# Kernel optimization log

Measured on AMD Instinct MI355X. Metric: run time of the kernel, lower is better.

Reference implementation:

```python
import jax, jax.numpy as jnp
import numpy as np
import math

B, S, D, H, HD, P = 2, 2048, 2048, 16, 128, 10
ROPE_BASE = 10000.0


def _rope_tables(seq_len, head_dim):
    inv_freq = 1.0 / (ROPE_BASE ** (np.arange(0, head_dim, 2, dtype=np.float32) / head_dim))
    t = np.arange(seq_len, dtype=np.float32)
    freqs = np.outer(t, inv_freq)                  # [S, hd/2]
    emb = np.concatenate([freqs, freqs], axis=-1)  # [S, hd]
    return jnp.asarray(np.cos(emb)), jnp.asarray(np.sin(emb))


def _rotate_half(x):
    half = x.shape[-1] // 2
    return jnp.concatenate([-x[..., half:], x[..., :half]], axis=-1)


def setup_inputs() -> dict:
    key = jax.random.key(0)
    ks = jax.random.split(key, 8)
    hidden_states = jax.random.normal(ks[0], (B, S, D), dtype=jnp.float32)
    # causal additive mask, llama convention: 0 where allowed, large negative above diagonal
    causal = jnp.triu(jnp.full((S, S), -1e9, dtype=jnp.float32), k=1)
    attention_mask = jnp.broadcast_to(causal[None, None], (B, 1, S, S))
    position_ids = jnp.broadcast_to(jnp.arange(S, dtype=jnp.int64)[None], (B, S))
    scale = 1.0 / math.sqrt(D)
    Wq = jax.random.normal(ks[1], (D, D), dtype=jnp.float32) * scale
    Wk = jax.random.normal(ks[2], (D, D), dtype=jnp.float32) * scale
    Wv = jax.random.normal(ks[3], (D, D), dtype=jnp.float32) * scale
    Wo = jax.random.normal(ks[4], (D, D), dtype=jnp.float32) * scale
    adapter_query = jax.random.normal(ks[5], (P, D), dtype=jnp.float32)
    adapter_gate = jax.random.normal(ks[6], (1, H, 1, 1), dtype=jnp.float32) * 0.1
    return dict(hidden_states=hidden_states, attention_mask=attention_mask,
                position_ids=position_ids, Wq=Wq, Wk=Wk, Wv=Wv, Wo=Wo,
                adapter_query=adapter_query, adapter_gate=adapter_gate)


def reference(hidden_states, attention_mask, position_ids, Wq, Wk, Wv, Wo,
              adapter_query, adapter_gate):
    bsz, q_len, _ = hidden_states.shape
    inv_sqrt_hd = 1.0 / math.sqrt(HD)

    def split_heads(x):  # [B,S,D] -> [B,H,S,hd]
        return x.reshape(bsz, q_len, H, HD).transpose(0, 2, 1, 3)

    q = split_heads(hidden_states @ Wq)
    k = split_heads(hidden_states @ Wk)
    v = split_heads(hidden_states @ Wv)

    # RoPE
    cos_t, sin_t = _rope_tables(q_len, HD)
    cos = cos_t[position_ids][:, None]  # [B,1,S,hd]
    sin = sin_t[position_ids][:, None]
    q = q * cos + _rotate_half(q) * sin
    k = k * cos + _rotate_half(k) * sin

    # main attention
    scores = jnp.einsum('bhqd,bhkd->bhqk', q, k) * inv_sqrt_hd
    scores = scores + attention_mask
    attn = jax.nn.softmax(scores.astype(jnp.float32), axis=-1).astype(q.dtype)
    attn_out = jnp.einsum('bhqk,bhkd->bhqd', attn, v)

    # adapter: soft prompt projected through k/v proj (learn_kv=False), no RoPE
    adapter = jnp.broadcast_to(adapter_query[None], (bsz, P, D))  # [B,P,D]
    a_k = (adapter @ Wk).reshape(bsz, P, H, HD).transpose(0, 2, 1, 3)  # [B,H,P,hd]
    a_v = (adapter @ Wv).reshape(bsz, P, H, HD).transpose(0, 2, 1, 3)
    a_scores = jnp.einsum('bhqd,bhpd->bhqp', q, a_k) * inv_sqrt_hd
    a_w = adapter_gate * jax.nn.softmax(a_scores.astype(jnp.float32), axis=-1).astype(q.dtype)
    a_out = jnp.einsum('bhqp,bhpd->bhqd', a_w, a_v)

    out = attn_out + a_out
    out = out.transpose(0, 2, 1, 3).reshape(bsz, q_len, D)
    return out @ Wo
```

## Files before the change

### kernel.cpp

```cpp
#include <hip/hip_runtime.h>
#include <cstdint>
#include <cstddef>

typedef __bf16 bf16x8 __attribute__((ext_vector_type(8)));
typedef float  f32x4  __attribute__((ext_vector_type(4)));

__device__ __forceinline__ unsigned short f2bf(float f) {
  unsigned int u = __float_as_uint(f);
  u += 0x7FFF + ((u >> 16) & 1);
  return (unsigned short)(u >> 16);
}
__device__ __forceinline__ float bf2f(unsigned short u) {
  return __uint_as_float(((unsigned int)u) << 16);
}

#define SEQ 2048
#define DMODEL 2048
#define NH 16
#define HD 128
#define NB 2
#define NP 10
#define MAUG 4106
#define SCALEL2 (0.08838834764831845f * 1.44269504088896340f)

#define GLOAD_LDS16(g, l) \
  __builtin_amdgcn_global_load_lds((__attribute__((address_space(1))) const void*)(g), \
                                   (__attribute__((address_space(3))) void*)(l), 16, 0, 0)

#define FENCE() asm volatile("" ::: "memory")
#define SBAR() do { FENCE(); __builtin_amdgcn_s_barrier(); FENCE(); } while (0)
#define WAITVM(N) asm volatile("s_waitcnt vmcnt(" #N ")" ::: "memory")

__global__ void k_tables(float* __restrict__ cost, float* __restrict__ sint) {
  int idx = blockIdx.x * 256 + threadIdx.x;
  if (idx >= SEQ * 64) return;
  int s = idx >> 6, i = idx & 63;
  double invf = exp(-((double)(2 * i) / 128.0) * log(10000.0));
  double a = (double)s * invf;
  float c = (float)cos(a), sn = (float)sin(a);
  cost[s * HD + i] = c;  cost[s * HD + 64 + i] = c;
  sint[s * HD + i] = sn; sint[s * HD + 64 + i] = sn;
}

__global__ __launch_bounds__(256) void k_wt(const float* __restrict__ W0,
                                            const float* __restrict__ W1,
                                            const float* __restrict__ W2,
                                            const float* __restrict__ W3,
                                            unsigned short* __restrict__ out) {
  __shared__ float tile[32][33];
  const float* W = (blockIdx.z == 0) ? W0 : (blockIdx.z == 1) ? W1 : (blockIdx.z == 2) ? W2 : W3;
  unsigned short* o = out + (size_t)blockIdx.z * DMODEL * DMODEL;
  int bx = blockIdx.x * 32, by = blockIdx.y * 32;
  int tx = threadIdx.x & 31, ty = threadIdx.x >> 5;
  #pragma unroll
  for (int j = 0; j < 32; j += 8)
    tile[ty + j][tx] = W[(size_t)(bx + ty + j) * DMODEL + by + tx];
  __syncthreads();
  #pragma unroll
  for (int j = 0; j < 32; j += 8)
    o[(size_t)(by + ty + j) * DMODEL + bx + tx] = f2bf(tile[tx][ty + j]);
}

__global__ void k_xaug(const float* __restrict__ X, const float* __restrict__ Aq,
                       unsigned short* __restrict__ xaug) {
  size_t idx = (size_t)blockIdx.x * 256 + threadIdx.x;
  if (idx >= (size_t)MAUG * DMODEL) return;
  size_t row = idx >> 11;
  int col = (int)(idx & 2047);
  float v = (row < (size_t)NB * SEQ) ? X[idx] : Aq[(row - NB * SEQ) * DMODEL + col];
  xaug[idx] = f2bf(v);
}

#define RD_A(dst, bb, MH) do { \
  _Pragma("unroll") for (int i_ = 0; i_ < 4; i_++) \
    _Pragma("unroll") for (int ks_ = 0; ks_ < 2; ks_++) \
      dst[i_][ks_] = *(const bf16x8*)&lds[(bb) + (wr*128 + (MH)*64 + i_*16 + lr)*64 + (((ks_*4+quad) ^ (lr & 7)) * 8)]; \
} while (0)

#define RD_B(dst, bb, NHH) do { \
  _Pragma("unroll") for (int j_ = 0; j_ < 2; j_++) \
    _Pragma("unroll") for (int ks_ = 0; ks_ < 2; ks_++) \
      dst[j_][ks_] = *(const bf16x8*)&lds[(bb) + 16384 + (wc*64 + (NHH)*32 + j_*16 + lr)*64 + (((ks_*4+quad) ^ (lr & 7)) * 8)]; \
} while (0)

#define MM(A, B, MH, NHH) do { \
  __builtin_amdgcn_s_setprio(1); \
  _Pragma("unroll") for (int i_ = 0; i_ < 4; i_++) \
    _Pragma("unroll") for (int j_ = 0; j_ < 2; j_++) { \
      acc[(MH)*4+i_][(NHH)*2+j_] = __builtin_amdgcn_mfma_f32_16x16x32_bf16(A[i_][0], B[j_][0], acc[(MH)*4+i_][(NHH)*2+j_], 0, 0, 0); \
      acc[(MH)*4+i_][(NHH)*2+j_] = __builtin_amdgcn_mfma_f32_16x16x32_bf16(A[i_][1], B[j_][1], acc[(MH)*4+i_][(NHH)*2+j_], 0, 0, 0); \
    } \
  __builtin_amdgcn_s_setprio(0); \
} while (0)

#define STG_AE(nb, ko) do { \
  GLOAD_LDS16(sA + (ko),                      &lds[(nb)*32768 + (qrow)*64 + g8]); \
  GLOAD_LDS16(sA + 128*(size_t)DMODEL + (ko), &lds[(nb)*32768 + (128+qrow)*64 + g8]); } while (0)
#define STG_AO(nb, ko) do { \
  GLOAD_LDS16(sA + 64*(size_t)DMODEL + (ko),  &lds[(nb)*32768 + (64+qrow)*64 + g8]); \
  GLOAD_LDS16(sA + 192*(size_t)DMODEL + (ko), &lds[(nb)*32768 + (192+qrow)*64 + g8]); } while (0)
#define STG_BE(nb, ko) do { \
  GLOAD_LDS16(sB + (ko),                      &lds[(nb)*32768 + 16384 + (qb)*64 + g8]); \
  GLOAD_LDS16(sB + 128*(size_t)DMODEL + (ko), &lds[(nb)*32768 + 16384 + (128+qb)*64 + g8]); } while (0)
#define STG_BO(nb, ko) do { \
  GLOAD_LDS16(sB + 32*(size_t)DMODEL + (ko),  &lds[(nb)*32768 + 16384 + (32+qb)*64 + g8]); \
  GLOAD_LDS16(sB + 160*(size_t)DMODEL + (ko), &lds[(nb)*32768 + 16384 + (160+qb)*64 + g8]); } while (0)

template<int BF16OUT>
__global__ __launch_bounds__(512, 2) void k_gemm256(const unsigned short* __restrict__ A,
                                                    const unsigned short* __restrict__ Bt,
                                                    void* __restrict__ Cv,
                                                    int M, size_t c_stride_mat) {
  __shared__ unsigned short lds[65536];
  const int t = threadIdx.x;
  const int lane = t & 63, w = t >> 6;
  const int lr = lane & 15, quad = lane >> 4;
  const int wr = w >> 2, wc = w & 3;
  const int tm = (M + 255) >> 8;
  const int perz = tm * 8;
  const int qchunk = gridDim.x >> 3;
  const int lin = ((int)blockIdx.x & 7) * qchunk + ((int)blockIdx.x >> 3);
  const int z = lin / perz;
  const int rem = lin - z * perz;
  const int m0 = (rem >> 3) * 256, n0 = (rem & 7) * 256;
  const unsigned short* Bz = Bt + (size_t)z * DMODEL * DMODEL;

  const int qrow = t >> 3;
  const int g8 = (t & 7) * 8;
  const int gsw8 = (((t & 7) ^ (qrow & 7)) * 8);
  const int qb = (qrow < 32) ? qrow : qrow + 32;

  const unsigned short* sA = A + (size_t)(m0 + qrow) * DMODEL + gsw8;
  const unsigned short* sB = Bz + (size_t)(n0 + qb) * DMODEL + gsw8;

  bf16x8 aE[4][2], aO[4][2], bE[2][2], bO[2][2];
  f32x4 acc[8][4];
  #pragma unroll
  for (int i = 0; i < 8; i++)
    #pragma unroll
    for (int j = 0; j < 4; j++) acc[i][j] = (f32x4){0.f, 0.f, 0.f, 0.f};

  STG_AE(0, 0); STG_BE(0, 0); STG_BO(0, 0); STG_AO(0, 0);
  WAITVM(4);
  SBAR();
  RD_A(aE, 0, 0); RD_B(bE, 0, 0);

  for (int kt = 0; kt < DMODEL / 64; kt++) {
    const int base = (kt & 1) << 15;
    const int nb2 = (kt & 1) ^ 1;
    const int nbase = nb2 << 15;
    const int ko = (kt + 1) * 64;
    const bool more = (kt + 1 < DMODEL / 64);

    if (more) { STG_AE(nb2, ko); WAITVM(4); } else WAITVM(2);
    SBAR();
    RD_B(bO, base, 1);
    MM(aE, bE, 0, 0);

    if (more) { STG_BE(nb2, ko); WAITVM(4); } else WAITVM(0);
    SBAR();
    RD_A(aO, base, 1);
    MM(aE, bO, 0, 1);

    if (more) STG_BO(nb2, ko);
    MM(aO, bE, 1, 0);

    if (more) {
      STG_AO(nb2, ko);
      WAITVM(4);
      SBAR();
      RD_A(aE, nbase, 0); RD_B(bE, nbase, 0);
    }
    MM(aO, bO, 1, 1);
  }

  #pragma unroll
  for (int mi = 0; mi < 8; mi++) {
    #pragma unroll
    for (int r = 0; r < 4; r++) {
      int row = m0 + wr * 128 + mi * 16 + quad * 4 + r;
      if (row < M) {
        if (BF16OUT) {
          unsigned short* C = (unsigned short*)Cv + (size_t)z * c_stride_mat;
          #pragma unroll
          for (int n = 0; n < 4; n++)
            C[(size_t)row * DMODEL + n0 + wc * 64 + n * 16 + lr] = f2bf(acc[mi][n][r]);
        } else {
          float* C = (float*)Cv + (size_t)z * c_stride_mat;
          #pragma unroll
          for (int n = 0; n < 4; n++)
            C[(size_t)row * DMODEL + n0 + wc * 64 + n * 16 + lr] = acc[mi][n][r];
        }
      }
    }
  }
}

#define O_LDA(MH) do { \
  _Pragma("unroll") for (int i_ = 0; i_ < 2; i_++) \
    _Pragma("unroll") for (int ks_ = 0; ks_ < 2; ks_++) \
      a[i_][ks_] = *(const bf16x8*)&lds[base + (wr*64 + ((MH)*2+i_)*16 + lr)*64 + (((ks_*4+quad) ^ (lr & 7)) * 8)]; \
} while (0)

#define O_LDB(NHH) do { \
  _Pragma("unroll") for (int j_ = 0; j_ < 2; j_++) \
    _Pragma("unroll") for (int ks_ = 0; ks_ < 2; ks_++) \
      b[(NHH)*2+j_][ks_] = *(const bf16x8*)&lds[base + 8192 + (wc*64 + ((NHH)*2+j_)*16 + lr)*64 + (((ks_*4+quad) ^ (lr & 7)) * 8)]; \
} while (0)

#define O_MFMA(MH, NHH) do { \
  __builtin_amdgcn_s_setprio(1); \
  _Pragma("unroll") for (int i_ = 0; i_ < 2; i_++) \
    _Pragma("unroll") for (int j_ = 0; j_ < 2; j_++) { \
      acc[(MH)*2+i_][(NHH)*2+j_] = __builtin_amdgcn_mfma_f32_16x16x32_bf16(a[i_][0], b[(NHH)*2+j_][0], acc[(MH)*2+i_][(NHH)*2+j_], 0, 0, 0); \
      acc[(MH)*2+i_][(NHH)*2+j_] = __builtin_amdgcn_mfma_f32_16x16x32_bf16(a[i_][1], b[(NHH)*2+j_][1], acc[(MH)*2+i_][(NHH)*2+j_], 0, 0, 0); \
    } \
  __builtin_amdgcn_s_setprio(0); \
} while (0)

#define O_STG_AE(nb, ko) GLOAD_LDS16(sA + (ko), &lds[(nb)*24576 + (qb)*64 + g8])
#define O_STG_AO(nb, ko) GLOAD_LDS16(sA + 32*(size_t)DMODEL + (ko), &lds[(nb)*24576 + (32+qb)*64 + g8])
#define O_STG_BE(nb, ko) do { \
  GLOAD_LDS16(sB + (ko),                      &lds[(nb)*24576 + 8192 + (qb)*64 + g8]); \
  GLOAD_LDS16(sB + 128*(size_t)DMODEL + (ko), &lds[(nb)*24576 + 8192 + (128+qb)*64 + g8]); } while (0)
#define O_STG_BO(nb, ko) do { \
  GLOAD_LDS16(sB + 32*(size_t)DMODEL + (ko),  &lds[(nb)*24576 + 8192 + (32+qb)*64 + g8]); \
  GLOAD_LDS16(sB + 160*(size_t)DMODEL + (ko), &lds[(nb)*24576 + 8192 + (160+qb)*64 + g8]); } while (0)

__global__ __launch_bounds__(512, 2) void k_gemmo(const unsigned short* __restrict__ A,
                                                  const unsigned short* __restrict__ Bt,
                                                  float* __restrict__ C) {
  __shared__ unsigned short lds[49152];
  const int t = threadIdx.x;
  const int lane = t & 63, w = t >> 6;
  const int lr = lane & 15, quad = lane >> 4;
  const int wr = w >> 2, wc = w & 3;
  const int lin = ((int)blockIdx.x & 7) * 32 + ((int)blockIdx.x >> 3);
  const int m0 = (lin >> 3) * 128, n0 = (lin & 7) * 256;

  const int qrow = t >> 3;
  const int g8 = (t & 7) * 8;
  const int gsw8 = (((t & 7) ^ (qrow & 7)) * 8);
  const int qb = (qrow < 32) ? qrow : qrow + 32;

  const unsigned short* sA = A + (size_t)(m0 + qb) * DMODEL + gsw8;
  const unsigned short* sB = Bt + (size_t)(n0 + qb) * DMODEL + gsw8;

  bf16x8 a[2][2], b[4][2];
  f32x4 acc[4][4];
  #pragma unroll
  for (int i = 0; i < 4; i++)
    #pragma unroll
    for (int j = 0; j < 4; j++) acc[i][j] = (f32x4){0.f, 0.f, 0.f, 0.f};

  O_STG_AE(0, 0); O_STG_BE(0, 0); O_STG_BO(0, 0); O_STG_AO(0, 0);
  WAITVM(3);
  SBAR();

  for (int kt = 0; kt < DMODEL / 64; kt++) {
    const int base = (kt & 1) * 24576;
    const int nb = (kt & 1) ^ 1;
    const int ko = (kt + 1) * 64;
    const bool more = (kt + 1 < DMODEL / 64);

    O_LDA(0);
    O_LDB(0);
    if (more) O_STG_AE(nb, ko);
    SBAR();
    O_MFMA(0, 0);
    if (more) WAITVM(2); else WAITVM(1);
    SBAR();

    O_LDB(1);
    if (more) O_STG_BE(nb, ko);
    SBAR();
    O_MFMA(0, 1);
    if (more) WAITVM(3); else WAITVM(0);
    SBAR();

    O_LDA(1);
    if (more) O_STG_BO(nb, ko);
    SBAR();
    O_MFMA(1, 0);
    SBAR();

    if (more) O_STG_AO(nb, ko);
    SBAR();
    O_MFMA(1, 1);
    if (more) WAITVM(3);
    SBAR();
  }

  #pragma unroll
  for (int mi = 0; mi < 4; mi++) {
    #pragma unroll
    for (int r = 0; r < 4; r++) {
      int row = m0 + wr * 64 + mi * 16 + quad * 4 + r;
      #pragma unroll
      for (int n = 0; n < 4; n++)
        C[(size_t)row * DMODEL + n0 + wc * 64 + n * 16 + lr] = acc[mi][n][r];
    }
  }
}

__global__ __launch_bounds__(256) void k_rope(const unsigned short* __restrict__ Qf,
                                              const unsigned short* __restrict__ Kf,
                                              const unsigned short* __restrict__ Vf,
                                              const float* __restrict__ cost, const float* __restrict__ sint,
                                              unsigned short* __restrict__ Qb, unsigned short* __restrict__ Kb,
                                              unsigned short* __restrict__ AKb, unsigned short* __restrict__ avt) {
  int row = blockIdx.x;
  int t = threadIdx.x;
  int c0 = t * 8;
  size_t off = (size_t)row * DMODEL + c0;
  if (row < NB * SEQ) {
    int s = row & (SEQ - 1);
    int d0 = c0 & (HD - 1);
    int po = (d0 < 64) ? 64 : -64;
    float sign = (d0 < 64) ? -1.f : 1.f;
    uint4 qv = *(const uint4*)&Qf[off];
    uint4 qp = *(const uint4*)&Qf[off + po];
    uint4 kv = *(const uint4*)&Kf[off];
    uint4 kp = *(const uint4*)&Kf[off + po];
    const unsigned short* qa = (const unsigned short*)&qv;
    const unsigned short* qb2 = (const unsigned short*)&qp;
    const unsigned short* ka = (const unsigned short*)&kv;
    const unsigned short* kb2 = (const unsigned short*)&kp;
    unsigned short oq[8], ok[8];
    #pragma unroll
    for (int j = 0; j < 8; j++) {
      float cv = cost[s * HD + d0 + j], sv = sint[s * HD + d0 + j];
      oq[j] = f2bf(bf2f(qa[j]) * cv + sign * bf2f(qb2[j]) * sv);
      ok[j] = f2bf(bf2f(ka[j]) * cv + sign * bf2f(kb2[j]) * sv);
    }
    *(uint4*)&Qb[off] = *(const uint4*)oq;
    *(uint4*)&Kb[off] = *(const uint4*)ok;
  } else {
    int p = row - NB * SEQ;
    uint4 kv = *(const uint4*)&Kf[off];
    uint4 vv = *(const uint4*)&Vf[off];
    *(uint4*)&AKb[(size_t)p * DMODEL + c0] = kv;
    const unsigned short* vp = (const unsigned short*)&vv;
    #pragma unroll
    for (int j = 0; j < 8; j++)
      avt[(size_t)(c0 + j) * 32 + p] = vp[j];
    if (p == 0) {
      #pragma unroll
      for (int j = 0; j < 8; j++)
        for (int pp = NP; pp < 32; pp++)
          avt[(size_t)(c0 + j) * 32 + pp] = 0;
    }
  }
}

__global__ __launch_bounds__(256) void k_vt(const unsigned short* __restrict__ Vf,
                                            unsigned short* __restrict__ Vt) {
  __shared__ unsigned short tile[64][72];
  const int t = threadIdx.x;
  int s0 = blockIdx.x * 64;
  int d0 = blockIdx.y * 64;
  int b = blockIdx.z >> 4, h = blockIdx.z & 15;
  #pragma unroll
  for (int j = t; j < 512; j += 256) {
    int row = j >> 3, ch = j & 7;
    *(uint4*)&tile[row][ch * 8] =
      *(const uint4*)&Vf[(size_t)(b * SEQ + s0 + row) * DMODEL + h * HD + d0 + ch * 8];
  }
  __syncthreads();
  #pragma unroll
  for (int j = t; j < 512; j += 256) {
    int dr = j >> 3, ch = j & 7;
    unsigned short tmp[8];
    #pragma unroll
    for (int k = 0; k < 8; k++) tmp[k] = tile[ch * 8 + k][dr];
    *(uint4*)&Vt[((size_t)((b * NH + h) * HD + d0 + dr)) * SEQ + s0 + ch * 8] = *(const uint4*)tmp;
  }
}

#define PSTR 68

__global__ __launch_bounds__(256, 2) void k_flash(const unsigned short* __restrict__ Qb,
                                               const unsigned short* __restrict__ Kb,
                                               const unsigned short* __restrict__ Vt,
                                               const unsigned short* __restrict__ AKb,
                                               const unsigned short* __restrict__ avt,
                                               const float* __restrict__ gate,
                                               unsigned short* __restrict__ Obuf,
                                               float* __restrict__ ml,
                                               unsigned short* __restrict__ Aout) {
  const int L = blockIdx.x;
  const int h = L & 15;
  const int slot = 39 - (L >> 4);
  const int b = blockIdx.y;
  int qt, j, P;
  if (slot < 4)       { qt = slot;               j = 0;          P = 1; }
  else if (slot < 12) { int s = slot - 4;  qt = 4 + (s >> 1);  j = s & 1; P = 2; }
  else if (slot < 24) { int s = slot - 12; qt = 8 + s / 3;     j = s % 3; P = 3; }
  else                { int s = slot - 24; qt = 12 + (s >> 2); j = s & 3; P = 4; }

  const int t = threadIdx.x, w = t >> 6, lane = t & 63;
  const int lr = lane & 15, quad = lane >> 4;

  __shared__ unsigned short Ks[2 * 64 * 128];
  __shared__ unsigned short Vs[128 * 64];
  __shared__ unsigned short Ps[4][32 * PSTR];
  unsigned short* Ps16 = &Ps[w][0];

  const int row_base = qt * 128 + w * 32;

  bf16x8 qf[2][4];
  #pragma unroll
  for (int mt = 0; mt < 2; mt++)
    #pragma unroll
    for (int kk = 0; kk < 4; kk++)
      qf[mt][kk] = *(const bf16x8*)&Qb[((size_t)(b * SEQ + row_base + mt * 16 + lr)) * DMODEL
                                       + h * HD + kk * 32 + quad * 8];

  f32x4 o[2][8];
  #pragma unroll
  for (int mt = 0; mt < 2; mt++)
    #pragma unroll
    for (int nt = 0; nt < 8; nt++) o[mt][nt] = (f32x4){0.f, 0.f, 0.f, 0.f};
  float l_i[2][4];
  #pragma unroll
  for (int mt = 0; mt < 2; mt++)
    #pragma unroll
    for (int r = 0; r < 4; r++) l_i[mt][r] = 0.f;

  const int krow = t >> 4;
  const int vd = t >> 3, vc = (t & 7) ^ (vd & 7);
  const int ktend = 2 * qt + 2;

  #pragma unroll
  for (int jj = 0; jj < 4; jj++) {
    int row = krow + jj * 16;
    int c = (t & 15) ^ (row & 15);
    GLOAD_LDS16(&Kb[((size_t)(b * SEQ + j * 64 + row)) * DMODEL + h * HD + c * 8],
                &Ks[(t + jj * 256) * 8]);
  }
  #pragma unroll
  for (int jj = 0; jj < 4; jj++) {
    int d = vd + jj * 32;
    GLOAD_LDS16(&Vt[((size_t)((b * NH + h) * HD + d)) * SEQ + j * 64 + vc * 8],
                &Vs[(t + jj * 256) * 8]);
  }

  int kb = 0;
  for (int kt = j; kt < ktend; kt += P) {
    const bool more = (kt + P < ktend);
    const int kbase = kb * 8192;
    const int nkbase = 8192 - kbase;

    WAITVM(4);
    SBAR();

    f32x4 s4[2][4];
    #pragma unroll
    for (int mt = 0; mt < 2; mt++)
      #pragma unroll
      for (int nt = 0; nt < 4; nt++) s4[mt][nt] = (f32x4){0.f, 0.f, 0.f, 0.f};
    #pragma unroll
    for (int nt = 0; nt < 4; nt++)
      #pragma unroll
      for (int kk = 0; kk < 4; kk++) {
        bf16x8 bv = *(const bf16x8*)&Ks[kbase + ((nt * 16 + lr) * 16 + ((kk * 4 + quad) ^ lr)) * 8];
        s4[0][nt] = __builtin_amdgcn_mfma_f32_16x16x32_bf16(qf[0][kk], bv, s4[0][nt], 0, 0, 0);
        s4[1][nt] = __builtin_amdgcn_mfma_f32_16x16x32_bf16(qf[1][kk], bv, s4[1][nt], 0, 0, 0);
      }

    if (more) {
      #pragma unroll
      for (int jj = 0; jj < 4; jj++) {
        int row = krow + jj * 16;
        int c = (t & 15) ^ (row & 15);
        GLOAD_LDS16(&Kb[((size_t)(b * SEQ + (kt + P) * 64 + row)) * DMODEL + h * HD + c * 8],
                    &Ks[nkbase + (t + jj * 256) * 8]);
      }
    }

    const int maybe_mask = (kt * 64 + 63 > row_base);
    #pragma unroll
    for (int mt = 0; mt < 2; mt++) {
      #pragma unroll
      for (int nt = 0; nt < 4; nt++) s4[mt][nt] = s4[mt][nt] * SCALEL2;
      if (maybe_mask) {
        #pragma unroll
        for (int nt = 0; nt < 4; nt++) {
          int col = kt * 64 + nt * 16 + lr;
          #pragma unroll
          for (int r = 0; r < 4; r++)
            if (col > row_base + mt * 16 + quad * 4 + r) s4[mt][nt][r] = -__builtin_inff();
        }
      }
      #pragma unroll
      for (int nt = 0; nt < 4; nt++)
        #pragma unroll
        for (int r = 0; r < 4; r++) {
          float p = __builtin_amdgcn_exp2f(s4[mt][nt][r]);
          l_i[mt][r] += p;
          Ps[w][(mt * 16 + quad * 4 + r) * PSTR + nt * 16 + lr] = f2bf(p);
        }
    }

    if (more) WAITVM(4); else WAITVM(0);
    SBAR();

    #pragma unroll
    for (int kk2 = 0; kk2 < 2; kk2++) {
      bf16x8 af0 = *(const bf16x8*)&Ps[w][(lr) * PSTR + kk2 * 32 + quad * 8];
      bf16x8 af1 = *(const bf16x8*)&Ps[w][(16 + lr) * PSTR + kk2 * 32 + quad * 8];
      #pragma unroll
      for (int nt = 0; nt < 8; nt++) {
        bf16x8 bv = *(const bf16x8*)&Vs[((nt * 16 + lr) * 8 + ((kk2 * 4 + quad) ^ (lr & 7))) * 8];
        o[0][nt] = __builtin_amdgcn_mfma_f32_16x16x32_bf16(af0, bv, o[0][nt], 0, 0, 0);
        o[1][nt] = __builtin_amdgcn_mfma_f32_16x16x32_bf16(af1, bv, o[1][nt], 0, 0, 0);
      }
    }

    SBAR();
    if (more) {
      #pragma unroll
      for (int jj = 0; jj < 4; jj++) {
        int d = vd + jj * 32;
        GLOAD_LDS16(&Vt[((size_t)((b * NH + h) * HD + d)) * SEQ + (kt + P) * 64 + vc * 8],
                    &Vs[(t + jj * 256) * 8]);
      }
    }
    kb ^= 1;
  }

  #pragma unroll
  for (int mt = 0; mt < 2; mt++)
    #pragma unroll
    for (int r = 0; r < 4; r++) {
      float l = l_i[mt][r];
      #pragma unroll
      for (int off = 1; off < 16; off <<= 1) l += __shfl_xor(l, off, 64);
      l_i[mt][r] = l;
    }

  const size_t slotg = (size_t)(b * 16 + h) * 40 + slot;

  if (j == 0) {
    const float g = gate[h];
    #pragma unroll
    for (int mt = 0; mt < 2; mt++) {
      f32x4 as4 = (f32x4){0.f, 0.f, 0.f, 0.f};
      #pragma unroll
      for (int kk = 0; kk < 4; kk++) {
        bf16x8 akf = *(const bf16x8*)&AKb[(size_t)lr * DMODEL + h * HD + kk * 32 + quad * 8];
        as4 = __builtin_amdgcn_mfma_f32_16x16x32_bf16(qf[mt][kk], akf, as4, 0, 0, 0);
      }
      as4 = as4 * SCALEL2;
      float al[4];
      #pragma unroll
      for (int r = 0; r < 4; r++) {
        float p = (lr < NP) ? __builtin_amdgcn_exp2f(as4[r]) : 0.f;
        as4[r] = p;
        float sum = p;
        #pragma unroll
        for (int off = 1; off < 16; off <<= 1) sum += __shfl_xor(sum, off, 64);
        al[r] = sum;
      }
      #pragma unroll
      for (int r = 0; r < 4; r++) {
        Ps[w][(mt * 16 + quad * 4 + r) * PSTR + lr] = f2bf(as4[r]);
        Ps[w][(mt * 16 + quad * 4 + r) * PSTR + 16 + lr] = 0;
      }
      bf16x8 af = *(const bf16x8*)&Ps[w][(mt * 16 + lr) * PSTR + quad * 8];
      f32x4 pa[8];
      #pragma unroll
      for (int nt = 0; nt < 8; nt++) {
        bf16x8 bv = *(const bf16x8*)&avt[(size_t)(h * HD + nt * 16 + lr) * 32 + quad * 8];
        pa[nt] = __builtin_amdgcn_mfma_f32_16x16x32_bf16(af, bv, (f32x4){0.f, 0.f, 0.f, 0.f}, 0, 0, 0);
      }
      float invla[4];
      #pragma unroll
      for (int r = 0; r < 4; r++) invla[r] = g / al[r];
      #pragma unroll
      for (int nt = 0; nt < 8; nt++)
        #pragma unroll
        for (int r = 0; r < 4; r++)
          Ps16[(quad * 4 + r) * 128 + nt * 16 + lr] = f2bf(pa[nt][r] * invla[r]);
      size_t gb = (((size_t)(b * 16 + h) * 16 + qt)) * 16384 + (size_t)(w * 32 + mt * 16) * 128;
      #pragma unroll
      for (int it = 0; it < 4; it++) {
        int i = lane + it * 64;
        int rr = i >> 4, ch = i & 15;
        *(uint4*)&Aout[gb + rr * 128 + ch * 8] = *(const uint4*)&Ps16[rr * 128 + ch * 8];
      }
    }
  }

  #pragma unroll
  for (int mt = 0; mt < 2; mt++) {
    if (lr == 0) {
      #pragma unroll
      for (int r = 0; r < 4; r++) {
        int rl = w * 32 + mt * 16 + quad * 4 + r;
        ml[slotg * 128 + rl] = l_i[mt][r];
      }
    }
    #pragma unroll
    for (int nt = 0; nt < 8; nt++)
      #pragma unroll
      for (int r = 0; r < 4; r++)
        Ps16[(quad * 4 + r) * 128 + nt * 16 + lr] = f2bf(o[mt][nt][r]);
    size_t gb = slotg * 16384 + (size_t)(w * 32 + mt * 16) * 128;
    #pragma unroll
    for (int it = 0; it < 4; it++) {
      int i = lane + it * 64;
      int rr = i >> 4, ch = i & 15;
      *(uint4*)&Obuf[gb + rr * 128 + ch * 8] = *(const uint4*)&Ps16[rr * 128 + ch * 8];
    }
  }
}

__global__ __launch_bounds__(256) void k_merge(const unsigned short* __restrict__ Obuf,
                                               const float* __restrict__ ml,
                                               const unsigned short* __restrict__ Aout,
                                               unsigned short* __restrict__ ab) {
  int idx = blockIdx.x * 256 + threadIdx.x;
  int ch = idx & 15;
  int row = (idx >> 4) & 2047;
  int h = (idx >> 15) & 15;
  int b = idx >> 19;
  int qt = row >> 7, rl = row & 127;
  int start = qt < 4 ? qt : qt < 8 ? 4 + 2 * (qt - 4) : qt < 12 ? 12 + 3 * (qt - 8) : 24 + 4 * (qt - 12);
  int P = qt < 4 ? 1 : qt < 8 ? 2 : qt < 12 ? 3 : 4;
  size_t sbase = (size_t)(b * 16 + h) * 40 + start;
  float den = 0.f;
  float acc[8] = {0.f, 0.f, 0.f, 0.f, 0.f, 0.f, 0.f, 0.f};
  #pragma unroll
  for (int jp = 0; jp < 4; jp++) {
    if (jp < P) {
      den += ml[(sbase + jp) * 128 + rl];
      uint4 ov = *(const uint4*)&Obuf[(sbase + jp) * 16384 + rl * 128 + ch * 8];
      const unsigned short* pv = (const unsigned short*)&ov;
      #pragma unroll
      for (int k = 0; k < 8; k++) acc[k] += bf2f(pv[k]);
    }
  }
  uint4 av = *(const uint4*)&Aout[(((size_t)(b * 16 + h) * 16 + qt)) * 16384 + rl * 128 + ch * 8];
  const unsigned short* pa = (const unsigned short*)&av;
  float dn = 1.0f / den;
  unsigned short res[8];
  #pragma unroll
  for (int k = 0; k < 8; k++) res[k] = f2bf(acc[k] * dn + bf2f(pa[k]));
  *(uint4*)&ab[((size_t)(b * 2048 + row)) * 2048 + h * 128 + ch * 8] = *(const uint4*)res;
}

extern "C" void kernel_launch(void* const* d_in, const int* in_sizes, int n_in,
                              void* d_out, int out_size, void* d_ws, size_t ws_size,
                              hipStream_t stream) {
  const float* hidden = (const float*)d_in[0];
  const float* Wq = (const float*)d_in[3];
  const float* Wk = (const float*)d_in[4];
  const float* Wv = (const float*)d_in[5];
  const float* Wo = (const float*)d_in[6];
  const float* Aq = (const float*)d_in[7];
  const float* gate = (const float*)d_in[8];
  float* out = (float*)d_out;

  char* ws = (char*)d_ws;
  size_t off = 0;
  auto alloc = [&](size_t bytes) -> void* {
    void* p = ws + off;
    off = (off + bytes + 255) & ~(size_t)255;
    return p;
  };
  unsigned short* wt   = (unsigned short*)alloc((size_t)4 * DMODEL * DMODEL * 2);
  unsigned short* xaug = (unsigned short*)alloc((size_t)MAUG * DMODEL * 2);
  unsigned short* qkvb = (unsigned short*)alloc((size_t)3 * MAUG * DMODEL * 2);
  unsigned short* qf = qkvb;
  unsigned short* kf = qkvb + (size_t)MAUG * DMODEL;
  unsigned short* vf = kf + (size_t)MAUG * DMODEL;
  unsigned short* qb  = (unsigned short*)alloc((size_t)NB * SEQ * DMODEL * 2);
  unsigned short* kb  = (unsigned short*)alloc((size_t)NB * SEQ * DMODEL * 2);
  unsigned short* vt  = (unsigned short*)alloc((size_t)NB * SEQ * DMODEL * 2);
  unsigned short* akb = (unsigned short*)alloc((size_t)16 * DMODEL * 2);
  unsigned short* avt = (unsigned short*)alloc((size_t)DMODEL * 32 * 2);
  float* cost = (float*)alloc((size_t)SEQ * HD * 4);
  float* sint = (float*)alloc((size_t)SEQ * HD * 4);
  unsigned short* obuf = (unsigned short*)alloc((size_t)NB * NH * 40 * 16384 * 2);
  float* mlb = (float*)alloc((size_t)NB * NH * 40 * 128 * 4);
  unsigned short* aout = (unsigned short*)alloc((size_t)NB * NH * 16 * 16384 * 2);
  unsigned short* ab = qf;

  k_tables<<<SEQ * 64 / 256, 256, 0, stream>>>(cost, sint);
  k_wt<<<dim3(64, 64, 4), 256, 0, stream>>>(Wq, Wk, Wv, Wo, wt);
  {
    size_t n = (size_t)MAUG * DMODEL;
    k_xaug<<<(unsigned)((n + 255) / 256), 256, 0, stream>>>(hidden, Aq, xaug);
  }
  k_gemm256<1><<<dim3(408), 512, 0, stream>>>(xaug, wt, qkvb, MAUG, (size_t)MAUG * DMODEL);
  k_rope<<<MAUG, 256, 0, stream>>>(qf, kf, vf, cost, sint, qb, kb, akb, avt);
  k_vt<<<dim3(32, 2, 32), 256, 0, stream>>>(vf, vt);
  k_flash<<<dim3(640, 2), 256, 0, stream>>>(qb, kb, vt, akb, avt, gate, obuf, mlb, aout);
  k_merge<<<4096, 256, 0, stream>>>(obuf, mlb, aout, ab);
  k_gemmo<<<dim3(256), 512, 0, stream>>>(ab, wt + (size_t)3 * DMODEL * DMODEL, out);
}
```

Baseline: 420.7 us.

## Vectorize prep kernels, merge rope and V transpose, use float RoPE tables

```diff
diff --git a/kernel.cpp b/kernel.cpp
--- a/kernel.cpp
+++ b/kernel.cpp
@@ -1,6 +1,7 @@
 #include <hip/hip_runtime.h>
 #include <cstdint>
 #include <cstddef>
+#include <cmath>
 
 typedef __bf16 bf16x8 __attribute__((ext_vector_type(8)));
 typedef float  f32x4  __attribute__((ext_vector_type(4)));
@@ -35,9 +36,9 @@
   int idx = blockIdx.x * 256 + threadIdx.x;
   if (idx >= SEQ * 64) return;
   int s = idx >> 6, i = idx & 63;
-  double invf = exp(-((double)(2 * i) / 128.0) * log(10000.0));
-  double a = (double)s * invf;
-  float c = (float)cos(a), sn = (float)sin(a);
+  float invf = expf(-((float)(2 * i) / 128.0f) * logf(10000.0f));
+  float a = (float)s * invf;
+  float c = cosf(a), sn = sinf(a);
   cost[s * HD + i] = c;  cost[s * HD + 64 + i] = c;
   sint[s * HD + i] = sn; sint[s * HD + 64 + i] = sn;
 }
@@ -47,28 +48,41 @@
                                             const float* __restrict__ W2,
                                             const float* __restrict__ W3,
                                             unsigned short* __restrict__ out) {
-  __shared__ float tile[32][33];
+  __shared__ float tile[64][65];
   const float* W = (blockIdx.z == 0) ? W0 : (blockIdx.z == 1) ? W1 : (blockIdx.z == 2) ? W2 : W3;
   unsigned short* o = out + (size_t)blockIdx.z * DMODEL * DMODEL;
-  int bx = blockIdx.x * 32, by = blockIdx.y * 32;
-  int tx = threadIdx.x & 31, ty = threadIdx.x >> 5;
-  #pragma unroll
-  for (int j = 0; j < 32; j += 8)
-    tile[ty + j][tx] = W[(size_t)(bx + ty + j) * DMODEL + by + tx];
+  int bx = blockIdx.x * 64, by = blockIdx.y * 64;
+  int c = threadIdx.x & 15, r0 = threadIdx.x >> 4;
+  #pragma unroll
+  for (int jj = 0; jj < 4; jj++) {
+    int r = r0 + jj * 16;
+    float4 v = *(const float4*)&W[(size_t)(bx + r) * DMODEL + by + c * 4];
+    tile[r][c * 4 + 0] = v.x; tile[r][c * 4 + 1] = v.y;
+    tile[r][c * 4 + 2] = v.z; tile[r][c * 4 + 3] = v.w;
+  }
   __syncthreads();
   #pragma unroll
-  for (int j = 0; j < 32; j += 8)
-    o[(size_t)(by + ty + j) * DMODEL + bx + tx] = f2bf(tile[tx][ty + j]);
+  for (int jj = 0; jj < 4; jj++) {
+    int ro = r0 + jj * 16;
+    unsigned short s4[4];
+    #pragma unroll
+    for (int k = 0; k < 4; k++) s4[k] = f2bf(tile[c * 4 + k][ro]);
+    *(uint2*)&o[(size_t)(by + ro) * DMODEL + bx + c * 4] = *(const uint2*)s4;
+  }
 }
 
 __global__ void k_xaug(const float* __restrict__ X, const float* __restrict__ Aq,
                        unsigned short* __restrict__ xaug) {
-  size_t idx = (size_t)blockIdx.x * 256 + threadIdx.x;
-  if (idx >= (size_t)MAUG * DMODEL) return;
-  size_t row = idx >> 11;
-  int col = (int)(idx & 2047);
-  float v = (row < (size_t)NB * SEQ) ? X[idx] : Aq[(row - NB * SEQ) * DMODEL + col];
-  xaug[idx] = f2bf(v);
+  size_t u = ((size_t)blockIdx.x * 256 + threadIdx.x) * 8;
+  size_t row = u >> 11;
+  int col = (int)(u & 2047);
+  const float* src = (row < (size_t)NB * SEQ) ? &X[u]
+                                              : &Aq[(row - NB * SEQ) * DMODEL + col];
+  float4 a = *(const float4*)src;
+  float4 b = *(const float4*)(src + 4);
+  unsigned short r[8] = { f2bf(a.x), f2bf(a.y), f2bf(a.z), f2bf(a.w),
+                          f2bf(b.x), f2bf(b.y), f2bf(b.z), f2bf(b.w) };
+  *(uint4*)&xaug[u] = *(const uint4*)r;
 }
 
 #define RD_A(dst, bb, MH) do { \
@@ -303,77 +317,79 @@
   }
 }
 
-__global__ __launch_bounds__(256) void k_rope(const unsigned short* __restrict__ Qf,
-                                              const unsigned short* __restrict__ Kf,
-                                              const unsigned short* __restrict__ Vf,
-                                              const float* __restrict__ cost, const float* __restrict__ sint,
-                                              unsigned short* __restrict__ Qb, unsigned short* __restrict__ Kb,
-                                              unsigned short* __restrict__ AKb, unsigned short* __restrict__ avt) {
-  int row = blockIdx.x;
-  int t = threadIdx.x;
-  int c0 = t * 8;
-  size_t off = (size_t)row * DMODEL + c0;
-  if (row < NB * SEQ) {
-    int s = row & (SEQ - 1);
-    int d0 = c0 & (HD - 1);
-    int po = (d0 < 64) ? 64 : -64;
-    float sign = (d0 < 64) ? -1.f : 1.f;
-    uint4 qv = *(const uint4*)&Qf[off];
-    uint4 qp = *(const uint4*)&Qf[off + po];
-    uint4 kv = *(const uint4*)&Kf[off];
-    uint4 kp = *(const uint4*)&Kf[off + po];
-    const unsigned short* qa = (const unsigned short*)&qv;
-    const unsigned short* qb2 = (const unsigned short*)&qp;
-    const unsigned short* ka = (const unsigned short*)&kv;
-    const unsigned short* kb2 = (const unsigned short*)&kp;
-    unsigned short oq[8], ok[8];
-    #pragma unroll
-    for (int j = 0; j < 8; j++) {
-      float cv = cost[s * HD + d0 + j], sv = sint[s * HD + d0 + j];
-      oq[j] = f2bf(bf2f(qa[j]) * cv + sign * bf2f(qb2[j]) * sv);
-      ok[j] = f2bf(bf2f(ka[j]) * cv + sign * bf2f(kb2[j]) * sv);
-    }
-    *(uint4*)&Qb[off] = *(const uint4*)oq;
-    *(uint4*)&Kb[off] = *(const uint4*)ok;
+__global__ __launch_bounds__(256) void k_ropevt(const unsigned short* __restrict__ Qf,
+                                                const unsigned short* __restrict__ Kf,
+                                                const unsigned short* __restrict__ Vf,
+                                                const float* __restrict__ cost, const float* __restrict__ sint,
+                                                unsigned short* __restrict__ Qb, unsigned short* __restrict__ Kb,
+                                                unsigned short* __restrict__ AKb, unsigned short* __restrict__ avt,
+                                                unsigned short* __restrict__ Vt) {
+  __shared__ unsigned short tile[64][72];
+  const int bid = blockIdx.x;
+  const int t = threadIdx.x;
+  if (bid < MAUG) {
+    int row = bid;
+    int c0 = t * 8;
+    size_t off = (size_t)row * DMODEL + c0;
+    if (row < NB * SEQ) {
+      int s = row & (SEQ - 1);
+      int d0 = c0 & (HD - 1);
+      int po = (d0 < 64) ? 64 : -64;
+      float sign = (d0 < 64) ? -1.f : 1.f;
+      uint4 qv = *(const uint4*)&Qf[off];
+      uint4 qp = *(const uint4*)&Qf[off + po];
+      uint4 kv = *(const uint4*)&Kf[off];
+      uint4 kp = *(const uint4*)&Kf[off + po];
+      const unsigned short* qa = (const unsigned short*)&qv;
+      const unsigned short* qb2 = (const unsigned short*)&qp;
+      const unsigned short* ka = (const unsigned short*)&kv;
+      const unsigned short* kb2 = (const unsigned short*)&kp;
+      unsigned short oq[8], ok[8];
+      #pragma unroll
+      for (int j = 0; j < 8; j++) {
+        float cv = cost[s * HD + d0 + j], sv = sint[s * HD + d0 + j];
+        oq[j] = f2bf(bf2f(qa[j]) * cv + sign * bf2f(qb2[j]) * sv);
+        ok[j] = f2bf(bf2f(ka[j]) * cv + sign * bf2f(kb2[j]) * sv);
+      }
+      *(uint4*)&Qb[off] = *(const uint4*)oq;
+      *(uint4*)&Kb[off] = *(const uint4*)ok;
+    } else {
+      int p = row - NB * SEQ;
+      uint4 kv = *(const uint4*)&Kf[off];
+      uint4 vv = *(const uint4*)&Vf[off];
+      *(uint4*)&AKb[(size_t)p * DMODEL + c0] = kv;
+      const unsigned short* vp = (const unsigned short*)&vv;
+      #pragma unroll
+      for (int j = 0; j < 8; j++)
+        avt[(size_t)(c0 + j) * 32 + p] = vp[j];
+      if (p == 0) {
+        #pragma unroll
+        for (int j = 0; j < 8; j++)
+          for (int pp = NP; pp < 32; pp++)
+            avt[(size_t)(c0 + j) * 32 + pp] = 0;
+      }
+    }
   } else {
-    int p = row - NB * SEQ;
-    uint4 kv = *(const uint4*)&Kf[off];
-    uint4 vv = *(const uint4*)&Vf[off];
-    *(uint4*)&AKb[(size_t)p * DMODEL + c0] = kv;
-    const unsigned short* vp = (const unsigned short*)&vv;
-    #pragma unroll
-    for (int j = 0; j < 8; j++)
-      avt[(size_t)(c0 + j) * 32 + p] = vp[j];
-    if (p == 0) {
-      #pragma unroll
-      for (int j = 0; j < 8; j++)
-        for (int pp = NP; pp < 32; pp++)
-          avt[(size_t)(c0 + j) * 32 + pp] = 0;
-    }
-  }
-}
-
-__global__ __launch_bounds__(256) void k_vt(const unsigned short* __restrict__ Vf,
-                                            unsigned short* __restrict__ Vt) {
-  __shared__ unsigned short tile[64][72];
-  const int t = threadIdx.x;
-  int s0 = blockIdx.x * 64;
-  int d0 = blockIdx.y * 64;
-  int b = blockIdx.z >> 4, h = blockIdx.z & 15;
-  #pragma unroll
-  for (int j = t; j < 512; j += 256) {
-    int row = j >> 3, ch = j & 7;
-    *(uint4*)&tile[row][ch * 8] =
-      *(const uint4*)&Vf[(size_t)(b * SEQ + s0 + row) * DMODEL + h * HD + d0 + ch * 8];
-  }
-  __syncthreads();
-  #pragma unroll
-  for (int j = t; j < 512; j += 256) {
-    int dr = j >> 3, ch = j & 7;
-    unsigned short tmp[8];
-    #pragma unroll
-    for (int k = 0; k < 8; k++) tmp[k] = tile[ch * 8 + k][dr];
-    *(uint4*)&Vt[((size_t)((b * NH + h) * HD + d0 + dr)) * SEQ + s0 + ch * 8] = *(const uint4*)tmp;
+    int b2 = bid - MAUG;
+    int s0 = (b2 & 31) * 64;
+    int d0 = ((b2 >> 5) & 1) * 64;
+    int z = b2 >> 6;
+    int b = z >> 4, h = z & 15;
+    #pragma unroll
+    for (int j = t; j < 512; j += 256) {
+      int row = j >> 3, ch = j & 7;
+      *(uint4*)&tile[row][ch * 8] =
+        *(const uint4*)&Vf[(size_t)(b * SEQ + s0 + row) * DMODEL + h * HD + d0 + ch * 8];
+    }
+    __syncthreads();
+    #pragma unroll
+    for (int j = t; j < 512; j += 256) {
+      int dr = j >> 3, ch = j & 7;
+      unsigned short tmp[8];
+      #pragma unroll
+      for (int k = 0; k < 8; k++) tmp[k] = tile[ch * 8 + k][dr];
+      *(uint4*)&Vt[((size_t)((b * NH + h) * HD + d0 + dr)) * SEQ + s0 + ch * 8] = *(const uint4*)tmp;
+    }
   }
 }
 
@@ -688,14 +704,10 @@
   unsigned short* ab = qf;
 
   k_tables<<<SEQ * 64 / 256, 256, 0, stream>>>(cost, sint);
-  k_wt<<<dim3(64, 64, 4), 256, 0, stream>>>(Wq, Wk, Wv, Wo, wt);
-  {
-    size_t n = (size_t)MAUG * DMODEL;
-    k_xaug<<<(unsigned)((n + 255) / 256), 256, 0, stream>>>(hidden, Aq, xaug);
-  }
+  k_wt<<<dim3(32, 32, 4), 256, 0, stream>>>(Wq, Wk, Wv, Wo, wt);
+  k_xaug<<<4106, 256, 0, stream>>>(hidden, Aq, xaug);
   k_gemm256<1><<<dim3(408), 512, 0, stream>>>(xaug, wt, qkvb, MAUG, (size_t)MAUG * DMODEL);
-  k_rope<<<MAUG, 256, 0, stream>>>(qf, kf, vf, cost, sint, qb, kb, akb, avt);
-  k_vt<<<dim3(32, 2, 32), 256, 0, stream>>>(vf, vt);
+  k_ropevt<<<MAUG + 2048, 256, 0, stream>>>(qf, kf, vf, cost, sint, qb, kb, akb, avt, vt);
   k_flash<<<dim3(640, 2), 256, 0, stream>>>(qb, kb, vt, akb, avt, gate, obuf, mlb, aout);
   k_merge<<<4096, 256, 0, stream>>>(obuf, mlb, aout, ab);
   k_gemmo<<<dim3(256), 512, 0, stream>>>(ab, wt + (size_t)3 * DMODEL * DMODEL, out);
```

After: 403.1 us. 4.2% less time.
